# Kernel tuning notes

Hardware: AMD Instinct MI355X
Metric: run time of the kernel (lower is better)

Reference implementation:

```python
import math
import jax, jax.numpy as jnp
import numpy as np

B, S, H = 2, 2048, 2048
N_HEADS, N_KV_HEADS = 16, 4
HEAD_DIM = H // N_HEADS  # 128
ROPE_BASE = 10000.0


def setup_inputs() -> dict:
    key = jax.random.key(0)
    ks = jax.random.split(key, 8)
    hidden_states = jax.random.normal(ks[0], (B, S, H), dtype=jnp.float32)
    # continuous, increasing timestamps in [0, S)
    time_values = jnp.sort(jax.random.uniform(ks[1], (B, S), dtype=jnp.float32) * S, axis=-1)
    sc = 1.0 / math.sqrt(H)
    wq = jax.random.normal(ks[2], (H, N_HEADS * HEAD_DIM), dtype=jnp.float32) * sc
    bq = jnp.zeros((N_HEADS * HEAD_DIM,), dtype=jnp.float32)
    wk = jax.random.normal(ks[3], (H, N_KV_HEADS * HEAD_DIM), dtype=jnp.float32) * sc
    bk = jnp.zeros((N_KV_HEADS * HEAD_DIM,), dtype=jnp.float32)
    wv = jax.random.normal(ks[4], (H, N_KV_HEADS * HEAD_DIM), dtype=jnp.float32) * sc
    bv = jnp.zeros((N_KV_HEADS * HEAD_DIM,), dtype=jnp.float32)
    wo = jax.random.normal(ks[5], (N_HEADS * HEAD_DIM, H), dtype=jnp.float32) * sc
    # learnable per-dimension frequency modulation (init ones, as in module)
    rope_w = jnp.ones((HEAD_DIM // 2,), dtype=jnp.float32)
    return {"hidden_states": hidden_states, "time_values": time_values,
            "wq": wq, "bq": bq, "wk": wk, "bk": bk, "wv": wv, "bv": bv,
            "wo": wo, "rope_w": rope_w}


def _rotate_half(x):
    x1, x2 = jnp.split(x, 2, axis=-1)
    return jnp.concatenate((-x2, x1), axis=-1)


def reference(hidden_states, time_values, wq, bq, wk, bk, wv, bv, wo, rope_w):
    b, s, h = hidden_states.shape
    # QKV projections -> [b, heads, s, head_dim]
    q = (hidden_states @ wq + bq).reshape(b, s, N_HEADS, HEAD_DIM).transpose(0, 2, 1, 3)
    k = (hidden_states @ wk + bk).reshape(b, s, N_KV_HEADS, HEAD_DIM).transpose(0, 2, 1, 3)
    v = (hidden_states @ wv + bv).reshape(b, s, N_KV_HEADS, HEAD_DIM).transpose(0, 2, 1, 3)
    # Continuous-time RoPE: freqs = t * inv_freq * w  -> [b, s, hd/2]
    inv_freq = 1.0 / (ROPE_BASE ** (jnp.arange(0, HEAD_DIM, 2, dtype=jnp.float32) / HEAD_DIM))
    freqs = time_values[:, :, None] * inv_freq * rope_w
    emb = jnp.concatenate((freqs, freqs), axis=-1)[:, None]  # [b, 1, s, hd]
    cos = jnp.cos(emb).astype(q.dtype)
    sin = jnp.sin(emb).astype(q.dtype)
    q = q * cos + _rotate_half(q) * sin
    k = k * cos + _rotate_half(k) * sin
    # GQA: repeat_kv
    n_rep = N_HEADS // N_KV_HEADS
    k = jnp.repeat(k, n_rep, axis=1)
    v = jnp.repeat(v, n_rep, axis=1)
    # scaled dot-product attention, causal
    scale = 1.0 / math.sqrt(HEAD_DIM)
    scores = jnp.einsum('bhqd,bhkd->bhqk', q, k) * scale
    causal = jnp.tril(jnp.ones((s, s), dtype=bool))
    scores = jnp.where(causal, scores, jnp.finfo(scores.dtype).min)
    attn = jax.nn.softmax(scores, axis=-1)
    out = jnp.einsum('bhqk,bhkd->bhqd', attn, v)  # [b, nh, s, hd]
    out = out.transpose(0, 2, 1, 3).reshape(b, s, N_HEADS * HEAD_DIM)
    return out @ wo
```

## Files before the change

kernel.cpp:

```cpp
#include <hip/hip_runtime.h>


#define S_LEN 2048
#define BATCH 2
#define NH    16
#define NKV   4
#define HD    128

typedef float  f32x4  __attribute__((ext_vector_type(4)));
typedef __bf16 bf16x8 __attribute__((ext_vector_type(8)));
typedef unsigned int u32x4 __attribute__((ext_vector_type(4)));
typedef unsigned int u32x2 __attribute__((ext_vector_type(2)));

__device__ inline unsigned short f2bf(float f) {
    unsigned u = __builtin_bit_cast(unsigned, f);
    unsigned r = (u + 0x7fffu + ((u >> 16) & 1u)) >> 16;
    return (unsigned short)r;
}

__device__ inline void gload_lds16(const void* g, void* l) {
    __builtin_amdgcn_global_load_lds(
        (const __attribute__((address_space(1))) unsigned int*)g,
        (__attribute__((address_space(3))) unsigned int*)l, 16, 0, 0);
}

__global__ void transpose_qkv(const float* __restrict__ wq,
                              const float* __restrict__ wk,
                              const float* __restrict__ wv,
                              unsigned short* __restrict__ Wt) {
    int z = blockIdx.z;
    const float* src = (z == 0) ? wq : ((z == 1) ? wk : wv);
    int C = (z == 0) ? 2048 : 512;
    long doff = (z == 0) ? 0L : ((z == 1) ? 2048L * 2048 : 2560L * 2048);
    int bx = blockIdx.x * 32, by = blockIdx.y * 32;
    if (bx >= C) return;
    __shared__ unsigned short t[32][33];
    int x = threadIdx.x, y0 = threadIdx.y;
    #pragma unroll
    for (int i = 0; i < 4; i++) {
        int y = y0 + i * 8;
        t[y][x] = f2bf(src[(long)(by + y) * C + bx + x]);
    }
    __syncthreads();
    #pragma unroll
    for (int i = 0; i < 4; i++) {
        int y = y0 + i * 8;
        Wt[doff + (long)(bx + y) * 2048 + by + x] = t[x][y];
    }
}

__global__ void transpose_to_bf16(const float* __restrict__ src,
                                  unsigned short* __restrict__ dst,
                                  int R, int C, long dst_off, int ldd) {
    __shared__ unsigned short t[32][33];
    int bx = blockIdx.x * 32, by = blockIdx.y * 32;
    int x = threadIdx.x, y0 = threadIdx.y;
    #pragma unroll
    for (int i = 0; i < 4; i++) {
        int y = y0 + i * 8;
        t[y][x] = f2bf(src[(long)(by + y) * C + bx + x]);
    }
    __syncthreads();
    #pragma unroll
    for (int i = 0; i < 4; i++) {
        int y = y0 + i * 8;
        dst[dst_off + (long)(bx + y) * ldd + by + x] = t[x][y];
    }
}

__global__ __launch_bounds__(256) void prep_kernel(
        const float* __restrict__ X, unsigned short* __restrict__ Xb,
        const float* __restrict__ bq, const float* __restrict__ bk,
        const float* __restrict__ bv, float* __restrict__ bsf,
        const float* __restrict__ tv, const float* __restrict__ rw,
        unsigned int* __restrict__ Tab) {
    int bi = blockIdx.x, tid = threadIdx.x;
    long i = ((long)bi * 256 + tid) * 8;
    {
        f32x4 a = *(const f32x4*)&X[i];
        f32x4 b = *(const f32x4*)&X[i + 4];
        u32x4 r;
        r.x = (unsigned)f2bf(a[0]) | ((unsigned)f2bf(a[1]) << 16);
        r.y = (unsigned)f2bf(a[2]) | ((unsigned)f2bf(a[3]) << 16);
        r.z = (unsigned)f2bf(b[0]) | ((unsigned)f2bf(b[1]) << 16);
        r.w = (unsigned)f2bf(b[2]) | ((unsigned)f2bf(b[3]) << 16);
        *(u32x4*)&Xb[i] = r;
    }
    if (bi < 12) {
        int ib = bi * 256 + tid;
        bsf[ib] = (ib < 2048) ? bq[ib] : ((ib < 2560) ? bk[ib - 2048] : bv[ib - 2560]);
    }
    if (bi < 1024) {
        int m = bi * 4 + (tid >> 6);
        int fi = tid & 63;
        float t = tv[m];
        float f = t * powf(10000.f, -(float)fi / 64.f) * rw[fi];
        Tab[m * 64 + fi] = (unsigned)f2bf(cosf(f)) | ((unsigned)f2bf(sinf(f)) << 16);
    }
}

__global__ __launch_bounds__(256) void gemm_qkv_rope(
        const unsigned short* __restrict__ A,
        const unsigned short* __restrict__ Bt,
        const float* __restrict__ bsf,
        const unsigned int* __restrict__ Tab,
        unsigned short* __restrict__ Qr,
        unsigned short* __restrict__ Kr,
        unsigned short* __restrict__ Vt) {
    __shared__ __align__(16) char smem[32 * 132 * 4];
    unsigned short* As = (unsigned short*)smem;
    unsigned short* Bs = (unsigned short*)(smem + 8192);
    float* Ep = (float*)smem;

    const int tid = threadIdx.x;
    const int wid = tid >> 6, lane = tid & 63, quad = lane >> 4, l16 = lane & 15;
    const int wr = wid >> 1, wc = wid & 1;
    const int m0 = blockIdx.y * 128, n0 = blockIdx.x * 128;
    const int bx = blockIdx.x;

    const int cA = tid, cB = 256 + tid;
    const int rowA = cA >> 2, octA = ((cA & 3) ^ ((cA >> 3) & 3)) * 8;
    const int rowB = cB >> 2, octB = ((cB & 3) ^ ((cB >> 3) & 3)) * 8;
    const int sw = (l16 >> 1) & 3;

    f32x4 acc[4][4];
    #pragma unroll
    for (int i = 0; i < 4; i++)
        #pragma unroll
        for (int j = 0; j < 4; j++)
            #pragma unroll
            for (int c = 0; c < 4; c++) acc[i][j][c] = 0.f;

    for (int k0 = 0; k0 < 2048; k0 += 32) {
        gload_lds16(&A[(long)(m0 + rowA) * 2048 + k0 + octA], &As[cA * 8]);
        gload_lds16(&A[(long)(m0 + rowB) * 2048 + k0 + octB], &As[cB * 8]);
        gload_lds16(&Bt[(long)(n0 + rowA) * 2048 + k0 + octA], &Bs[cA * 8]);
        gload_lds16(&Bt[(long)(n0 + rowB) * 2048 + k0 + octB], &Bs[cB * 8]);
        __syncthreads();
        bf16x8 af[4], bfr[4];
        #pragma unroll
        for (int mi = 0; mi < 4; mi++)
            af[mi] = *(const bf16x8*)
                &As[(wr * 64 + mi * 16 + l16) * 32 + ((quad ^ sw)) * 8];
        #pragma unroll
        for (int ni = 0; ni < 4; ni++)
            bfr[ni] = *(const bf16x8*)
                &Bs[(wc * 64 + ni * 16 + l16) * 32 + ((quad ^ sw)) * 8];
        #pragma unroll
        for (int mi = 0; mi < 4; mi++)
            #pragma unroll
            for (int ni = 0; ni < 4; ni++)
                acc[mi][ni] = __builtin_amdgcn_mfma_f32_16x16x32_bf16(
                    af[mi], bfr[ni], acc[mi][ni], 0, 0, 0);
        __syncthreads();
    }

    float bv4[4];
    #pragma unroll
    for (int ni = 0; ni < 4; ni++) bv4[ni] = bsf[n0 + wc * 64 + ni * 16 + l16];
    const bool isV = (bx >= 20);
    const float qs = (bx < 16) ? (0.08838834764831845f * 1.4426950408889634f) : 1.0f;

    const int lr = tid >> 3, jj = tid & 7, j0 = jj * 8;

    u32x4 tq[4][2];
    if (!isV) {
        #pragma unroll
        for (int mi = 0; mi < 4; mi++) {
            int gm = m0 + ((lr >> 4) << 6) + mi * 16 + (lr & 15);
            tq[mi][0] = *(const u32x4*)&Tab[(long)gm * 64 + j0];
            tq[mi][1] = *(const u32x4*)&Tab[(long)gm * 64 + j0 + 4];
        }
    }

    #pragma unroll
    for (int mi = 0; mi < 4; mi++) {
        #pragma unroll
        for (int ni = 0; ni < 4; ni++)
            #pragma unroll
            for (int r = 0; r < 4; r++)
                Ep[(wr * 16 + quad * 4 + r) * 132 + wc * 64 + ni * 16 + l16] =
                    acc[mi][ni][r] + bv4[ni];
        __syncthreads();
        if (!isV) {
            const int gm = m0 + ((lr >> 4) << 6) + mi * 16 + (lr & 15);
            const int bb = gm >> 11, s = gm & 2047;
            unsigned short* dst = (bx < 16)
                ? Qr + ((long)(bb * NH + bx) * S_LEN + s) * HD
                : Kr + ((long)(bb * NKV + (bx - 16)) * S_LEN + s) * HD;
            f32x4 x1a = *(f32x4*)&Ep[lr * 132 + j0];
            f32x4 x1b = *(f32x4*)&Ep[lr * 132 + j0 + 4];
            f32x4 x2a = *(f32x4*)&Ep[lr * 132 + 64 + j0];
            f32x4 x2b = *(f32x4*)&Ep[lr * 132 + 64 + j0 + 4];
            f32x4 la, lb, ha, hb;
            #pragma unroll
            for (int e = 0; e < 4; e++) {
                float ca = __builtin_bit_cast(float, tq[mi][0][e] << 16);
                float sa = __builtin_bit_cast(float, tq[mi][0][e] & 0xffff0000u);
                float cb = __builtin_bit_cast(float, tq[mi][1][e] << 16);
                float sb = __builtin_bit_cast(float, tq[mi][1][e] & 0xffff0000u);
                la[e] = (x1a[e] * ca - x2a[e] * sa) * qs;
                ha[e] = (x2a[e] * ca + x1a[e] * sa) * qs;
                lb[e] = (x1b[e] * cb - x2b[e] * sb) * qs;
                hb[e] = (x2b[e] * cb + x1b[e] * sb) * qs;
            }
            u32x4 lo, hi;
            lo.x = (unsigned)f2bf(la[0]) | ((unsigned)f2bf(la[1]) << 16);
            lo.y = (unsigned)f2bf(la[2]) | ((unsigned)f2bf(la[3]) << 16);
            lo.z = (unsigned)f2bf(lb[0]) | ((unsigned)f2bf(lb[1]) << 16);
            lo.w = (unsigned)f2bf(lb[2]) | ((unsigned)f2bf(lb[3]) << 16);
            hi.x = (unsigned)f2bf(ha[0]) | ((unsigned)f2bf(ha[1]) << 16);
            hi.y = (unsigned)f2bf(ha[2]) | ((unsigned)f2bf(ha[3]) << 16);
            hi.z = (unsigned)f2bf(hb[0]) | ((unsigned)f2bf(hb[1]) << 16);
            hi.w = (unsigned)f2bf(hb[2]) | ((unsigned)f2bf(hb[3]) << 16);
            *(u32x4*)&dst[j0] = lo;
            *(u32x4*)&dst[64 + j0] = hi;
        } else {
            const int d = tid >> 1, sh = tid & 1;
            const int gmb = m0 + sh * 64 + mi * 16;
            const int bb = gmb >> 11, s0 = gmb & 2047;
            unsigned short* dst =
                Vt + ((long)(bb * NKV + (bx - 20)) * HD + d) * S_LEN + s0;
            unsigned short pv[16];
            #pragma unroll
            for (int t = 0; t < 16; t++)
                pv[t] = f2bf(Ep[(sh * 16 + t) * 132 + d]);
            u32x4 v0, v1;
            v0.x = (unsigned)pv[0]  | ((unsigned)pv[1]  << 16);
            v0.y = (unsigned)pv[2]  | ((unsigned)pv[3]  << 16);
            v0.z = (unsigned)pv[4]  | ((unsigned)pv[5]  << 16);
            v0.w = (unsigned)pv[6]  | ((unsigned)pv[7]  << 16);
            v1.x = (unsigned)pv[8]  | ((unsigned)pv[9]  << 16);
            v1.y = (unsigned)pv[10] | ((unsigned)pv[11] << 16);
            v1.z = (unsigned)pv[12] | ((unsigned)pv[13] << 16);
            v1.w = (unsigned)pv[14] | ((unsigned)pv[15] << 16);
            *(u32x4*)&dst[0] = v0;
            *(u32x4*)&dst[8] = v1;
        }
        __syncthreads();
    }
}

template <typename CT>
__global__ __launch_bounds__(256) void gemm_bt_async(
        const unsigned short* __restrict__ A,
        const unsigned short* __restrict__ Bt,
        CT* __restrict__ C,
        const float* __restrict__ bias,
        int K, int lda, int ldb, int ldc) {
    __shared__ __align__(16) unsigned short As[128 * 32];
    __shared__ __align__(16) unsigned short Bs[128 * 32];
    const int tid = threadIdx.x;
    const int wid = tid >> 6, lane = tid & 63, quad = lane >> 4, l16 = lane & 15;
    const int wr = wid >> 1, wc = wid & 1;
    const int m0 = blockIdx.y * 128, n0 = blockIdx.x * 128;

    const int cA = tid, cB = 256 + tid;
    const int rowA = cA >> 2, octA = ((cA & 3) ^ ((cA >> 3) & 3)) * 8;
    const int rowB = cB >> 2, octB = ((cB & 3) ^ ((cB >> 3) & 3)) * 8;
    const int sw = (l16 >> 1) & 3;

    f32x4 acc[4][4];
    #pragma unroll
    for (int i = 0; i < 4; i++)
        #pragma unroll
        for (int j = 0; j < 4; j++)
            #pragma unroll
            for (int c = 0; c < 4; c++) acc[i][j][c] = 0.f;

    for (int k0 = 0; k0 < K; k0 += 32) {
        gload_lds16(&A[(long)(m0 + rowA) * lda + k0 + octA], &As[cA * 8]);
        gload_lds16(&A[(long)(m0 + rowB) * lda + k0 + octB], &As[cB * 8]);
        gload_lds16(&Bt[(long)(n0 + rowA) * ldb + k0 + octA], &Bs[cA * 8]);
        gload_lds16(&Bt[(long)(n0 + rowB) * ldb + k0 + octB], &Bs[cB * 8]);
        __syncthreads();
        bf16x8 af[4], bfr[4];
        #pragma unroll
        for (int mi = 0; mi < 4; mi++)
            af[mi] = *(const bf16x8*)
                &As[(wr * 64 + mi * 16 + l16) * 32 + (quad ^ sw) * 8];
        #pragma unroll
        for (int ni = 0; ni < 4; ni++)
            bfr[ni] = *(const bf16x8*)
                &Bs[(wc * 64 + ni * 16 + l16) * 32 + (quad ^ sw) * 8];
        #pragma unroll
        for (int mi = 0; mi < 4; mi++)
            #pragma unroll
            for (int ni = 0; ni < 4; ni++)
                acc[mi][ni] = __builtin_amdgcn_mfma_f32_16x16x32_bf16(
                    af[mi], bfr[ni], acc[mi][ni], 0, 0, 0);
        __syncthreads();
    }

    #pragma unroll
    for (int mi = 0; mi < 4; mi++) {
        #pragma unroll
        for (int ni = 0; ni < 4; ni++) {
            int gn = n0 + wc * 64 + ni * 16 + l16;
            float bv_ = bias ? bias[gn] : 0.f;
            #pragma unroll
            for (int r = 0; r < 4; r++) {
                int gm = m0 + wr * 64 + mi * 16 + quad * 4 + r;
                float v = acc[mi][ni][r] + bv_;
                if constexpr (sizeof(CT) == 4) C[(long)gm * ldc + gn] = v;
                else                           C[(long)gm * ldc + gn] = f2bf(v);
            }
        }
    }
}

__global__ __launch_bounds__(512, 4) void attn_kernel(
        const unsigned short* __restrict__ Qr,
        const unsigned short* __restrict__ Kr,
        const unsigned short* __restrict__ Vt,
        unsigned short* __restrict__ Out) {
    __shared__ __align__(16) unsigned short Ks[64 * 128];
    __shared__ __align__(16) unsigned short Vs[128 * 64];
    __shared__ __align__(16) unsigned short Ps[8][16 * 68];

    const int h = blockIdx.x, b = blockIdx.z;
    const int qt = b ? blockIdx.y : (int)(gridDim.y - 1 - blockIdx.y);
    const int tid = threadIdx.x, w = tid >> 6, lane = tid & 63;
    const int quad = lane >> 4, l16 = lane & 15;
    const int hk = h >> 2;
    const unsigned short* Qb = Qr + (long)((b * NH + h) * S_LEN) * HD;
    const unsigned short* Kb = Kr + (long)((b * NKV + hk) * S_LEN) * HD;
    const unsigned short* Vb = Vt + (long)((b * NKV + hk) * HD) * S_LEN;
    const int qw = qt * 128 + w * 16;
    const int q  = qw + l16;
    const float MASK_MIN = -3.0e38f;

    bf16x8 qf[4];
    #pragma unroll
    for (int kc = 0; kc < 4; kc++)
        qf[kc] = *(const bf16x8*)&Qb[(long)q * HD + kc * 32 + quad * 8];

    f32x4 o[8];
    #pragma unroll
    for (int db = 0; db < 8; db++)
        #pragma unroll
        for (int c = 0; c < 4; c++) o[db][c] = 0.f;
    float mr = MASK_MIN, lr = 0.f;

    const int sK0 = tid, sK1 = tid + 512;
    const int kR0 = sK0 >> 4, kC0 = ((sK0 & 15) ^ (kR0 & 15)) * 8;
    const int kR1 = sK1 >> 4, kC1 = ((sK1 & 15) ^ (kR1 & 15)) * 8;
    const int vR0 = sK0 >> 3, vC0 = ((sK0 & 7) ^ (vR0 & 7)) * 8;
    const int vR1 = sK1 >> 3, vC1 = ((sK1 & 7) ^ (vR1 & 7)) * 8;

    const int nkt = 2 * qt + 2;
    for (int kt = 0; kt < nkt; kt++) {
        const int k0 = kt * 64;
        __syncthreads();
        gload_lds16(&Kb[(long)(k0 + kR0) * HD + kC0], &Ks[sK0 * 8]);
        gload_lds16(&Kb[(long)(k0 + kR1) * HD + kC1], &Ks[sK1 * 8]);
        gload_lds16(&Vb[(long)vR0 * S_LEN + k0 + vC0], &Vs[sK0 * 8]);
        gload_lds16(&Vb[(long)vR1 * S_LEN + k0 + vC1], &Vs[sK1 * 8]);
        __syncthreads();

        if (k0 > qw + 15) continue;

        f32x4 sc[4];
        #pragma unroll
        for (int nb = 0; nb < 4; nb++) {
            #pragma unroll
            for (int c = 0; c < 4; c++) sc[nb][c] = 0.f;
            #pragma unroll
            for (int kc = 0; kc < 4; kc++) {
                bf16x8 kf = *(const bf16x8*)
                    &Ks[(nb * 16 + l16) * 128 + (((kc * 4 + quad) ^ l16) * 8)];
                sc[nb] = __builtin_amdgcn_mfma_f32_16x16x32_bf16(kf, qf[kc], sc[nb], 0, 0, 0);
            }
        }
        if (k0 + 63 > qw) {
            #pragma unroll
            for (int nb = 0; nb < 4; nb++) {
                int kvb = k0 + nb * 16 + quad * 4;
                #pragma unroll
                for (int r = 0; r < 4; r++)
                    sc[nb][r] = (kvb + r > q) ? MASK_MIN : sc[nb][r];
            }
        }
        float tm = MASK_MIN;
        #pragma unroll
        for (int nb = 0; nb < 4; nb++)
            #pragma unroll
            for (int r = 0; r < 4; r++) tm = fmaxf(tm, sc[nb][r]);
        tm = fmaxf(tm, __shfl_xor(tm, 16));
        tm = fmaxf(tm, __shfl_xor(tm, 32));
        float mn = fmaxf(mr, tm);
        float alpha = exp2f(mr - mn);
        mr = mn;
        float rs = 0.f;
        #pragma unroll
        for (int nb = 0; nb < 4; nb++) {
            float pv0 = exp2f(sc[nb][0] - mn), pv1 = exp2f(sc[nb][1] - mn);
            float pv2 = exp2f(sc[nb][2] - mn), pv3 = exp2f(sc[nb][3] - mn);
            rs += (pv0 + pv1) + (pv2 + pv3);
            u32x2 pk;
            pk.x = (unsigned)f2bf(pv0) | ((unsigned)f2bf(pv1) << 16);
            pk.y = (unsigned)f2bf(pv2) | ((unsigned)f2bf(pv3) << 16);
            *(u32x2*)&Ps[w][l16 * 68 + nb * 16 + quad * 4] = pk;
        }
        rs += __shfl_xor(rs, 16);
        rs += __shfl_xor(rs, 32);
        lr = lr * alpha + rs;
        #pragma unroll
        for (int db = 0; db < 8; db++)
            #pragma unroll
            for (int c = 0; c < 4; c++) o[db][c] *= alpha;

        #pragma unroll
        for (int kk = 0; kk < 2; kk++) {
            bf16x8 pf = *(const bf16x8*)&Ps[w][l16 * 68 + kk * 32 + quad * 8];
            #pragma unroll
            for (int db = 0; db < 8; db++) {
                bf16x8 vf = *(const bf16x8*)
                    &Vs[(db * 16 + l16) * 64 + (((kk * 4 + quad) ^ (l16 & 7)) * 8)];
                o[db] = __builtin_amdgcn_mfma_f32_16x16x32_bf16(vf, pf, o[db], 0, 0, 0);
            }
        }
    }

    float inv_l = 1.0f / lr;
    long obase = (long)(b * S_LEN + q) * 2048 + h * 128 + quad * 4;
    #pragma unroll
    for (int db = 0; db < 8; db++) {
        u32x2 pk;
        pk.x = (unsigned)f2bf(o[db][0] * inv_l) | ((unsigned)f2bf(o[db][1] * inv_l) << 16);
        pk.y = (unsigned)f2bf(o[db][2] * inv_l) | ((unsigned)f2bf(o[db][3] * inv_l) << 16);
        *(u32x2*)&Out[obase + db * 16] = pk;
    }
}

extern "C" void kernel_launch(void* const* d_in, const int* in_sizes, int n_in,
                              void* d_out, int out_size, void* d_ws, size_t ws_size,
                              hipStream_t stream) {
    const float* X  = (const float*)d_in[0];
    const float* tv = (const float*)d_in[1];
    const float* wq = (const float*)d_in[2];
    const float* bq = (const float*)d_in[3];
    const float* wk = (const float*)d_in[4];
    const float* bk = (const float*)d_in[5];
    const float* wv = (const float*)d_in[6];
    const float* bv = (const float*)d_in[7];
    const float* wo = (const float*)d_in[8];
    const float* rw = (const float*)d_in[9];

    char* ws = (char*)d_ws;
    unsigned short* Wt  = (unsigned short*)ws; ws += 3072L * 2048 * 2;
    float*          bsf = (float*)ws;          ws += 3072L * 4;
    unsigned int*   Tab = (unsigned int*)ws;   ws += 4096L * 64 * 4;
    unsigned short* Qr  = (unsigned short*)ws; ws += (long)BATCH * NH  * S_LEN * HD * 2;
    unsigned short* Kr  = (unsigned short*)ws; ws += (long)BATCH * NKV * S_LEN * HD * 2;
    unsigned short* Vt  = (unsigned short*)ws; ws += (long)BATCH * NKV * HD * S_LEN * 2;
    unsigned short* AO  = (unsigned short*)ws; ws += 4096L * 2048 * 2;
    unsigned short* Xb  = AO;

    transpose_qkv<<<dim3(64, 64, 3), dim3(32, 8), 0, stream>>>(wq, wk, wv, Wt);
    prep_kernel<<<4096, 256, 0, stream>>>(X, Xb, bq, bk, bv, bsf, tv, rw, Tab);
    gemm_qkv_rope<<<dim3(24, 32), 256, 0, stream>>>(Xb, Wt, bsf, Tab, Qr, Kr, Vt);
    transpose_to_bf16<<<dim3(64, 64), dim3(32, 8), 0, stream>>>(wo, Wt, 2048, 2048, 0L, 2048);
    attn_kernel<<<dim3(NH, S_LEN / 128, BATCH), 512, 0, stream>>>(Qr, Kr, Vt, AO);
    gemm_bt_async<float><<<dim3(16, 32), 256, 0, stream>>>(
        AO, Wt, (float*)d_out, nullptr, 2048, 2048, 2048, 2048);
}
```

Baseline: 343.7 us.

## Deepen GEMM K-tile to 64, skip redundant softmax rescale, use native bf16 converts

Both GEMM kernels now stage 64-wide K slices per iteration instead of 32, using an 8-way XOR swizzle. This halves the number of barrier pairs and gives each wave more MFMAs per sync, at the cost of doubling LDS use per block, which may reduce occupancy. The attention kernel skips the running-max rescale of the accumulator when no lane's max increased, using a wave-uniform __any check. It also replaces manual bf16 rounding with native __bf16 conversions for the P tile and the output stores.

```diff
diff --git a/kernel.cpp b/kernel.cpp
--- a/kernel.cpp
+++ b/kernel.cpp
@@ -9,6 +9,7 @@
 
 typedef float  f32x4  __attribute__((ext_vector_type(4)));
 typedef __bf16 bf16x8 __attribute__((ext_vector_type(8)));
+typedef __bf16 bf16x4 __attribute__((ext_vector_type(4)));
 typedef unsigned int u32x4 __attribute__((ext_vector_type(4)));
 typedef unsigned int u32x2 __attribute__((ext_vector_type(2)));
 
@@ -107,9 +108,9 @@
         unsigned short* __restrict__ Qr,
         unsigned short* __restrict__ Kr,
         unsigned short* __restrict__ Vt) {
-    __shared__ __align__(16) char smem[32 * 132 * 4];
+    __shared__ __align__(16) char smem[32768];
     unsigned short* As = (unsigned short*)smem;
-    unsigned short* Bs = (unsigned short*)(smem + 8192);
+    unsigned short* Bs = (unsigned short*)(smem + 16384);
     float* Ep = (float*)smem;
 
     const int tid = threadIdx.x;
@@ -117,11 +118,7 @@
     const int wr = wid >> 1, wc = wid & 1;
     const int m0 = blockIdx.y * 128, n0 = blockIdx.x * 128;
     const int bx = blockIdx.x;
-
-    const int cA = tid, cB = 256 + tid;
-    const int rowA = cA >> 2, octA = ((cA & 3) ^ ((cA >> 3) & 3)) * 8;
-    const int rowB = cB >> 2, octB = ((cB & 3) ^ ((cB >> 3) & 3)) * 8;
-    const int sw = (l16 >> 1) & 3;
+    const int l7 = l16 & 7;
 
     f32x4 acc[4][4];
     #pragma unroll
@@ -131,27 +128,38 @@
             #pragma unroll
             for (int c = 0; c < 4; c++) acc[i][j][c] = 0.f;
 
-    for (int k0 = 0; k0 < 2048; k0 += 32) {
-        gload_lds16(&A[(long)(m0 + rowA) * 2048 + k0 + octA], &As[cA * 8]);
-        gload_lds16(&A[(long)(m0 + rowB) * 2048 + k0 + octB], &As[cB * 8]);
-        gload_lds16(&Bt[(long)(n0 + rowA) * 2048 + k0 + octA], &Bs[cA * 8]);
-        gload_lds16(&Bt[(long)(n0 + rowB) * 2048 + k0 + octB], &Bs[cB * 8]);
-        __syncthreads();
-        bf16x8 af[4], bfr[4];
-        #pragma unroll
-        for (int mi = 0; mi < 4; mi++)
-            af[mi] = *(const bf16x8*)
-                &As[(wr * 64 + mi * 16 + l16) * 32 + ((quad ^ sw)) * 8];
-        #pragma unroll
-        for (int ni = 0; ni < 4; ni++)
-            bfr[ni] = *(const bf16x8*)
-                &Bs[(wc * 64 + ni * 16 + l16) * 32 + ((quad ^ sw)) * 8];
-        #pragma unroll
-        for (int mi = 0; mi < 4; mi++)
+    for (int k0 = 0; k0 < 2048; k0 += 64) {
+        #pragma unroll
+        for (int i = 0; i < 4; i++) {
+            int c = tid + 256 * i;
+            int row = c >> 3, loct = ((c & 7) ^ (row & 7)) * 8;
+            gload_lds16(&A[(long)(m0 + row) * 2048 + k0 + loct], &As[c * 8]);
+        }
+        #pragma unroll
+        for (int i = 0; i < 4; i++) {
+            int c = tid + 256 * i;
+            int row = c >> 3, loct = ((c & 7) ^ (row & 7)) * 8;
+            gload_lds16(&Bt[(long)(n0 + row) * 2048 + k0 + loct], &Bs[c * 8]);
+        }
+        __syncthreads();
+        #pragma unroll
+        for (int s = 0; s < 2; s++) {
+            bf16x8 af[4], bfr[4];
+            #pragma unroll
+            for (int mi = 0; mi < 4; mi++)
+                af[mi] = *(const bf16x8*)
+                    &As[(wr * 64 + mi * 16 + l16) * 64 + (((s * 4 + quad) ^ l7)) * 8];
             #pragma unroll
             for (int ni = 0; ni < 4; ni++)
-                acc[mi][ni] = __builtin_amdgcn_mfma_f32_16x16x32_bf16(
-                    af[mi], bfr[ni], acc[mi][ni], 0, 0, 0);
+                bfr[ni] = *(const bf16x8*)
+                    &Bs[(wc * 64 + ni * 16 + l16) * 64 + (((s * 4 + quad) ^ l7)) * 8];
+            #pragma unroll
+            for (int mi = 0; mi < 4; mi++)
+                #pragma unroll
+                for (int ni = 0; ni < 4; ni++)
+                    acc[mi][ni] = __builtin_amdgcn_mfma_f32_16x16x32_bf16(
+                        af[mi], bfr[ni], acc[mi][ni], 0, 0, 0);
+        }
         __syncthreads();
     }
 
@@ -248,17 +256,13 @@
         CT* __restrict__ C,
         const float* __restrict__ bias,
         int K, int lda, int ldb, int ldc) {
-    __shared__ __align__(16) unsigned short As[128 * 32];
-    __shared__ __align__(16) unsigned short Bs[128 * 32];
+    __shared__ __align__(16) unsigned short As[128 * 64];
+    __shared__ __align__(16) unsigned short Bs[128 * 64];
     const int tid = threadIdx.x;
     const int wid = tid >> 6, lane = tid & 63, quad = lane >> 4, l16 = lane & 15;
     const int wr = wid >> 1, wc = wid & 1;
     const int m0 = blockIdx.y * 128, n0 = blockIdx.x * 128;
-
-    const int cA = tid, cB = 256 + tid;
-    const int rowA = cA >> 2, octA = ((cA & 3) ^ ((cA >> 3) & 3)) * 8;
-    const int rowB = cB >> 2, octB = ((cB & 3) ^ ((cB >> 3) & 3)) * 8;
-    const int sw = (l16 >> 1) & 3;
+    const int l7 = l16 & 7;
 
     f32x4 acc[4][4];
     #pragma unroll
@@ -268,27 +272,38 @@
             #pragma unroll
             for (int c = 0; c < 4; c++) acc[i][j][c] = 0.f;
 
-    for (int k0 = 0; k0 < K; k0 += 32) {
-        gload_lds16(&A[(long)(m0 + rowA) * lda + k0 + octA], &As[cA * 8]);
-        gload_lds16(&A[(long)(m0 + rowB) * lda + k0 + octB], &As[cB * 8]);
-        gload_lds16(&Bt[(long)(n0 + rowA) * ldb + k0 + octA], &Bs[cA * 8]);
-        gload_lds16(&Bt[(long)(n0 + rowB) * ldb + k0 + octB], &Bs[cB * 8]);
-        __syncthreads();
-        bf16x8 af[4], bfr[4];
-        #pragma unroll
-        for (int mi = 0; mi < 4; mi++)
-            af[mi] = *(const bf16x8*)
-                &As[(wr * 64 + mi * 16 + l16) * 32 + (quad ^ sw) * 8];
-        #pragma unroll
-        for (int ni = 0; ni < 4; ni++)
-            bfr[ni] = *(const bf16x8*)
-                &Bs[(wc * 64 + ni * 16 + l16) * 32 + (quad ^ sw) * 8];
-        #pragma unroll
-        for (int mi = 0; mi < 4; mi++)
+    for (int k0 = 0; k0 < K; k0 += 64) {
+        #pragma unroll
+        for (int i = 0; i < 4; i++) {
+            int c = tid + 256 * i;
+            int row = c >> 3, loct = ((c & 7) ^ (row & 7)) * 8;
+            gload_lds16(&A[(long)(m0 + row) * lda + k0 + loct], &As[c * 8]);
+        }
+        #pragma unroll
+        for (int i = 0; i < 4; i++) {
+            int c = tid + 256 * i;
+            int row = c >> 3, loct = ((c & 7) ^ (row & 7)) * 8;
+            gload_lds16(&Bt[(long)(n0 + row) * ldb + k0 + loct], &Bs[c * 8]);
+        }
+        __syncthreads();
+        #pragma unroll
+        for (int s = 0; s < 2; s++) {
+            bf16x8 af[4], bfr[4];
+            #pragma unroll
+            for (int mi = 0; mi < 4; mi++)
+                af[mi] = *(const bf16x8*)
+                    &As[(wr * 64 + mi * 16 + l16) * 64 + (((s * 4 + quad) ^ l7)) * 8];
             #pragma unroll
             for (int ni = 0; ni < 4; ni++)
-                acc[mi][ni] = __builtin_amdgcn_mfma_f32_16x16x32_bf16(
-                    af[mi], bfr[ni], acc[mi][ni], 0, 0, 0);
+                bfr[ni] = *(const bf16x8*)
+                    &Bs[(wc * 64 + ni * 16 + l16) * 64 + (((s * 4 + quad) ^ l7)) * 8];
+            #pragma unroll
+            for (int mi = 0; mi < 4; mi++)
+                #pragma unroll
+                for (int ni = 0; ni < 4; ni++)
+                    acc[mi][ni] = __builtin_amdgcn_mfma_f32_16x16x32_bf16(
+                        af[mi], bfr[ni], acc[mi][ni], 0, 0, 0);
+        }
         __syncthreads();
     }
 
@@ -388,27 +403,30 @@
             for (int r = 0; r < 4; r++) tm = fmaxf(tm, sc[nb][r]);
         tm = fmaxf(tm, __shfl_xor(tm, 16));
         tm = fmaxf(tm, __shfl_xor(tm, 32));
-        float mn = fmaxf(mr, tm);
-        float alpha = exp2f(mr - mn);
-        mr = mn;
+
+        float mn = mr;
+        if (__any(tm > mr)) {
+            mn = fmaxf(mr, tm);
+            float alpha = exp2f(mr - mn);
+            mr = mn;
+            lr *= alpha;
+            #pragma unroll
+            for (int db = 0; db < 8; db++)
+                #pragma unroll
+                for (int c = 0; c < 4; c++) o[db][c] *= alpha;
+        }
         float rs = 0.f;
         #pragma unroll
         for (int nb = 0; nb < 4; nb++) {
             float pv0 = exp2f(sc[nb][0] - mn), pv1 = exp2f(sc[nb][1] - mn);
             float pv2 = exp2f(sc[nb][2] - mn), pv3 = exp2f(sc[nb][3] - mn);
             rs += (pv0 + pv1) + (pv2 + pv3);
-            u32x2 pk;
-            pk.x = (unsigned)f2bf(pv0) | ((unsigned)f2bf(pv1) << 16);
-            pk.y = (unsigned)f2bf(pv2) | ((unsigned)f2bf(pv3) << 16);
-            *(u32x2*)&Ps[w][l16 * 68 + nb * 16 + quad * 4] = pk;
+            bf16x4 pk4 = { (__bf16)pv0, (__bf16)pv1, (__bf16)pv2, (__bf16)pv3 };
+            *(bf16x4*)&Ps[w][l16 * 68 + nb * 16 + quad * 4] = pk4;
         }
         rs += __shfl_xor(rs, 16);
         rs += __shfl_xor(rs, 32);
-        lr = lr * alpha + rs;
-        #pragma unroll
-        for (int db = 0; db < 8; db++)
-            #pragma unroll
-            for (int c = 0; c < 4; c++) o[db][c] *= alpha;
+        lr += rs;
 
         #pragma unroll
         for (int kk = 0; kk < 2; kk++) {
@@ -426,10 +444,9 @@
     long obase = (long)(b * S_LEN + q) * 2048 + h * 128 + quad * 4;
     #pragma unroll
     for (int db = 0; db < 8; db++) {
-        u32x2 pk;
-        pk.x = (unsigned)f2bf(o[db][0] * inv_l) | ((unsigned)f2bf(o[db][1] * inv_l) << 16);
-        pk.y = (unsigned)f2bf(o[db][2] * inv_l) | ((unsigned)f2bf(o[db][3] * inv_l) << 16);
-        *(u32x2*)&Out[obase + db * 16] = pk;
+        bf16x4 pk4 = { (__bf16)(o[db][0] * inv_l), (__bf16)(o[db][1] * inv_l),
+                       (__bf16)(o[db][2] * inv_l), (__bf16)(o[db][3] * inv_l) };
+        *(bf16x4*)&Out[obase + db * 16] = pk4;
     }
 }
 
```

Result: faster. 325.8 us (-5.2%).
